# Kernel optimization log

Hardware: AMD Instinct MI355X
Metric: run time of the kernel (lower is better)

## Reference

```python
import jax, jax.numpy as jnp
import numpy as np

# SHOT descriptor hyperparameters (match init_kwargs defaults)
K_LRF = 16        # neighbors_for_lrf
A_BINS = 8        # azimuth bins
E_BINS = 2        # elevation bins
R_BINS = 2        # radial bins
H_BINS = 11       # cosine-histogram bins
EPS = 1e-8


def knn_shot_lrf(vertices, k):
    """vertices: (N,3). Returns lrfs (N,3,3) with column 0 = normal,
    neighborhoods (N,k,3) relative coords, neighbor indices (N,k)."""
    # Pairwise squared distances (N,N) -- dominant memory-bound intermediate.
    d2 = jnp.sum((vertices[:, None, :] - vertices[None, :, :]) ** 2, axis=-1)
    neg_d2, idx = jax.lax.top_k(-d2, k)                 # k nearest (incl. self)
    dists = jnp.sqrt(jnp.maximum(-neg_d2, 0.0))         # (N,k)
    neighborhoods = vertices[idx] - vertices[:, None, :]  # (N,k,3)

    # SHOT local reference frame: distance-weighted covariance + eigh.
    radius = dists[:, -1]                                # (N,) support radius
    w = jnp.maximum(radius[:, None] - dists, 0.0)        # (N,k)
    cov = jnp.einsum('nk,nki,nkj->nij', w, neighborhoods, neighborhoods)
    cov = cov / (jnp.sum(w, axis=-1)[:, None, None] + EPS)
    _, evecs = jnp.linalg.eigh(cov)                      # ascending eigenvalues
    n = evecs[..., 0]                                    # normal: smallest eval
    x = evecs[..., 2]                                    # x-axis: largest eval

    # Sign disambiguation: orient each axis with the majority of neighbors.
    proj_n = jnp.einsum('nki,ni->nk', neighborhoods, n)
    n = n * jnp.where(jnp.sum(jnp.sign(proj_n), axis=-1) >= 0, 1.0, -1.0)[:, None]
    proj_x = jnp.einsum('nki,ni->nk', neighborhoods, x)
    x = x * jnp.where(jnp.sum(jnp.sign(proj_x), axis=-1) >= 0, 1.0, -1.0)[:, None]
    y = jnp.cross(n, x)
    lrfs = jnp.stack([n, x, y], axis=-1)                 # lrfs[..., 0] = normal
    return lrfs, neighborhoods, idx


def shot_descr(neighborhoods, normals, neighborhood_indices, radius):
    """Spherical-grid (azimuth x elevation x radial) histograms of normal cosines."""
    N, k, _ = neighborhoods.shape
    nbr_normals = normals[neighborhood_indices]          # (N,k,3) irregular gather
    cos = jnp.clip(jnp.einsum('ni,nki->nk', normals, nbr_normals), -1.0, 1.0)

    r = jnp.linalg.norm(neighborhoods, axis=-1)          # (N,k)
    xg, yg, zg = neighborhoods[..., 0], neighborhoods[..., 1], neighborhoods[..., 2]

    az = jnp.arctan2(yg, xg)                                             # [-pi, pi]
    az_bin = jnp.clip(((az + jnp.pi) / (2.0 * jnp.pi) * A_BINS).astype(jnp.int32), 0, A_BINS - 1)
    el = (zg / (r + EPS) + 1.0) * 0.5                                    # [0, 1]
    el_bin = jnp.clip((el * E_BINS).astype(jnp.int32), 0, E_BINS - 1)
    rad_bin = jnp.clip((r / (radius + EPS) * R_BINS).astype(jnp.int32), 0, R_BINS - 1)
    h_bin = jnp.clip(((cos + 1.0) * 0.5 * H_BINS).astype(jnp.int32), 0, H_BINS - 1)

    flat = ((az_bin * E_BINS + el_bin) * R_BINS + rad_bin) * H_BINS + h_bin  # (N,k)
    mask = (r <= radius).astype(neighborhoods.dtype)

    total = A_BINS * E_BINS * R_BINS * H_BINS
    descr = jnp.zeros((N, total), neighborhoods.dtype)
    descr = descr.at[jnp.arange(N)[:, None], flat].add(mask)             # scatter-add
    return descr / (jnp.linalg.norm(descr, axis=-1, keepdims=True) + EPS)


def _one_cloud(vertices):
    lrfs, nbh, idx = knn_shot_lrf(vertices, K_LRF)
    # sphere_radius == 0.0 branch: global max neighborhood extent
    radius = jnp.max(jnp.linalg.norm(nbh, axis=-1))
    return shot_descr(nbh, lrfs[..., 0], idx, radius)


def setup_inputs() -> dict:
    key = jax.random.key(0)
    vertices = jax.random.normal(key, (8, 4096, 3), dtype=jnp.float32)
    return {"vertices": vertices}


def reference(vertices):
    # (B, N, 3) -> (B, N, 352)
    return jax.vmap(_one_cloud)(vertices)
```

## Files before the change

### kernel.cpp

```cpp
#include <hip/hip_runtime.h>
#include <math.h>

#define NPTS 4096
#define KNN 16
#define TBINS 352
#define PPB 16
#define CITER (NPTS / 16)
#define CAP 96
#define BINOFF 210
#define HROW 68

__device__ __forceinline__ void ins16(unsigned long long* K, unsigned long long key) {
  if (key < K[15]) {
#pragma unroll
    for (int q = 15; q >= 1; --q) {
      bool ltm = key < K[q - 1];
      bool ltk = key < K[q];
      K[q] = ltm ? K[q - 1] : (ltk ? key : K[q]);
    }
    if (key < K[0]) K[0] = key;
  }
}

#define JROT(App, Aqq, Apq, Arp, Arq, V0p, V0q, V1p, V1q, V2p, V2q)            \
  do {                                                                         \
    double apq_ = Apq;                                                         \
    if (fabs(apq_) > 1e-300) {                                                 \
      double tau_ = (Aqq - App) / (2.0 * apq_);                                \
      double t_ = (tau_ >= 0.0) ? 1.0 / (tau_ + sqrt(1.0 + tau_ * tau_))       \
                                : 1.0 / (tau_ - sqrt(1.0 + tau_ * tau_));      \
      double c_ = 1.0 / sqrt(1.0 + t_ * t_);                                   \
      double s_ = t_ * c_;                                                     \
      App = App - t_ * apq_;                                                   \
      Aqq = Aqq + t_ * apq_;                                                   \
      Apq = 0.0;                                                               \
      double u_, w_;                                                           \
      u_ = Arp; w_ = Arq; Arp = c_ * u_ - s_ * w_; Arq = s_ * u_ + c_ * w_;    \
      u_ = V0p; w_ = V0q; V0p = c_ * u_ - s_ * w_; V0q = s_ * u_ + c_ * w_;    \
      u_ = V1p; w_ = V1q; V1p = c_ * u_ - s_ * w_; V1q = s_ * u_ + c_ * w_;    \
      u_ = V2p; w_ = V2q; V2p = c_ * u_ - s_ * w_; V2q = s_ * u_ + c_ * w_;    \
    }                                                                          \
  } while (0)

__global__ __launch_bounds__(256, 2) void knn_select_kernel(
    const float* __restrict__ verts,
    int* __restrict__ nbr_idx,
    unsigned int* __restrict__ rad2_bits)
{
  __shared__ unsigned char hist[256 * HROW];
  __shared__ unsigned short ptot[PPB][64];
  __shared__ unsigned long long surv[PPB][CAP];
  __shared__ unsigned int scnt[PPB];
  __shared__ unsigned int tbl[PPB];
  __shared__ unsigned int radsh[PPB];

  const int blk = blockIdx.x;
  const int cloud = blk >> 8;
  const int pbase = (blk & 255) * PPB;
  const float* __restrict__ vb = verts + (size_t)cloud * NPTS * 3;
  const int tid = (int)threadIdx.x;

  {
    unsigned int* h32 = (unsigned int*)hist;
#pragma unroll
    for (int k = 0; k < 17; ++k) h32[tid * 17 + k] = 0u;
  }
  if (tid < PPB) scnt[tid] = 0u;
  __syncthreads();

  const int p = tid >> 4;
  const int c = tid & 15;
  const int i = pbase + p;
  const float xi = vb[3 * i + 0], yi = vb[3 * i + 1], zi = vb[3 * i + 2];

#pragma unroll 4
  for (int s = 0; s < CITER; ++s) {
    const int j = (s << 4) | c;
    const float* vp = vb + 3 * j;
    float dx = __fsub_rn(vp[0], xi);
    float dy = __fsub_rn(vp[1], yi);
    float dz = __fsub_rn(vp[2], zi);
    float d2 = __fadd_rn(__fadd_rn(__fmul_rn(dx, dx), __fmul_rn(dy, dy)),
                         __fmul_rn(dz, dz));
    int b = (int)(__float_as_uint(d2) >> 22) - BINOFF;
    b = min(max(b, 0), 63);
    hist[tid * HROW + b] += (unsigned char)1;
  }
  __syncthreads();

#pragma unroll
  for (int bq = 0; bq < 4; ++bq) {
    int b = 4 * c + bq;
    unsigned int tot = 0;
    for (int r = 0; r < 16; ++r) tot += hist[(p * 16 + r) * HROW + b];
    ptot[p][b] = (unsigned short)tot;
  }
  __syncthreads();

  if (c == 0) {
    unsigned int cum = 0; int B = 63;
    for (int b = 0; b < 64; ++b) {
      cum += ptot[p][b];
      if (cum >= KNN) { B = b; break; }
    }
    tbl[p] = (B >= 63) ? 0xFFFFFFFFu : ((unsigned int)(B + 1 + BINOFF) << 22);
  }
  __syncthreads();

  {
    const unsigned int T = tbl[p];
#pragma unroll 4
    for (int s = 0; s < CITER; ++s) {
      const int j = (s << 4) | c;
      const float* vp = vb + 3 * j;
      float dx = __fsub_rn(vp[0], xi);
      float dy = __fsub_rn(vp[1], yi);
      float dz = __fsub_rn(vp[2], zi);
      float d2 = __fadd_rn(__fadd_rn(__fmul_rn(dx, dx), __fmul_rn(dy, dy)),
                           __fmul_rn(dz, dz));
      unsigned int bits = __float_as_uint(d2);
      if (bits < T) {
        unsigned int pos = atomicAdd(&scnt[p], 1u);
        if (pos < CAP) surv[p][pos] = ((unsigned long long)bits << 32) | (unsigned int)j;
      }
    }
  }
  __syncthreads();

  if (c == 0) {
    unsigned long long K[KNN];
#pragma unroll
    for (int k = 0; k < KNN; ++k) K[k] = 0xFFFFFFFFFFFFFFFFull;
    const int n = (int)scnt[p];
    if (n <= CAP) {
      for (int t = 0; t < n; ++t) ins16(K, surv[p][t]);
    } else {
      for (int j = 0; j < NPTS; ++j) {
        const float* vp = vb + 3 * j;
        float dx = __fsub_rn(vp[0], xi);
        float dy = __fsub_rn(vp[1], yi);
        float dz = __fsub_rn(vp[2], zi);
        float d2 = __fadd_rn(__fadd_rn(__fmul_rn(dx, dx), __fmul_rn(dy, dy)),
                             __fmul_rn(dz, dz));
        ins16(K, ((unsigned long long)__float_as_uint(d2) << 32) | (unsigned int)j);
      }
    }
    const int gp = cloud * NPTS + i;
#pragma unroll
    for (int k = 0; k < KNN; ++k) nbr_idx[gp * KNN + k] = (int)(K[k] & 0xFFFFFFFFull);
    radsh[p] = (unsigned int)(K[KNN - 1] >> 32);
  }
  __syncthreads();

  if (tid == 0) {
    unsigned int m = radsh[0];
#pragma unroll
    for (int q = 1; q < PPB; ++q) m = max(m, radsh[q]);
    atomicMax(&rad2_bits[cloud], m);
  }
}

__global__ __launch_bounds__(256, 1) void normal_kernel(
    const float* __restrict__ verts,
    const int* __restrict__ nbr_idx,
    float* __restrict__ normals)
{
  const int t = blockIdx.x * 256 + (int)threadIdx.x;
  const int gp = t >> 4;
  const int c = t & 15;
  const int cloud = gp >> 12;
  const int i = gp & (NPTS - 1);
  const float* __restrict__ vb = verts + (size_t)cloud * NPTS * 3;
  const float xi = vb[3 * i + 0], yi = vb[3 * i + 1], zi = vb[3 * i + 2];

  const int id = nbr_idx[gp * KNN + c];
  const float* vp = vb + 3 * id;
  const float dx = __fsub_rn(vp[0], xi);
  const float dy = __fsub_rn(vp[1], yi);
  const float dz = __fsub_rn(vp[2], zi);
  const float d2 = __fadd_rn(__fadd_rn(__fmul_rn(dx, dx), __fmul_rn(dy, dy)),
                             __fmul_rn(dz, dz));
  const double dist = sqrt((double)d2);
  const double radius_i = __shfl(dist, 15, 16);

  double w = radius_i - dist;
  if (w < 0.0) w = 0.0;
  const double dxd = (double)dx, dyd = (double)dy, dzd = (double)dz;
  const double wx = w * dxd, wy = w * dyd;
  double c00 = wx * dxd, c01 = wx * dyd, c02 = wx * dzd;
  double c11 = wy * dyd, c12 = wy * dzd, c22 = (w * dzd) * dzd;
  double sw = w;

#pragma unroll
  for (int m = 8; m >= 1; m >>= 1) {
    c00 += __shfl_xor(c00, m);
    c01 += __shfl_xor(c01, m);
    c02 += __shfl_xor(c02, m);
    c11 += __shfl_xor(c11, m);
    c12 += __shfl_xor(c12, m);
    c22 += __shfl_xor(c22, m);
    sw  += __shfl_xor(sw,  m);
  }

  const double inv = 1.0 / (sw + 1e-8);
  c00 *= inv; c01 *= inv; c02 *= inv; c11 *= inv; c12 *= inv; c22 *= inv;

  double A00 = c00, A01 = c01, A02 = c02, A11 = c11, A12 = c12, A22 = c22;
  double v00 = 1, v01 = 0, v02 = 0,
         v10 = 0, v11 = 1, v12 = 0,
         v20 = 0, v21 = 0, v22 = 1;
  for (int sweep = 0; sweep < 8; ++sweep) {
    JROT(A00, A11, A01, A02, A12, v00, v01, v10, v11, v20, v21);
    JROT(A00, A22, A02, A01, A12, v00, v02, v10, v12, v20, v22);
    JROT(A11, A22, A12, A01, A02, v01, v02, v11, v12, v21, v22);
  }

  double nx, ny, nz;
  if (A00 <= A11 && A00 <= A22)      { nx = v00; ny = v10; nz = v20; }
  else if (A11 <= A22)               { nx = v01; ny = v11; nz = v21; }
  else                               { nx = v02; ny = v12; nz = v22; }
  const double rn = 1.0 / sqrt(nx * nx + ny * ny + nz * nz);
  nx *= rn; ny *= rn; nz *= rn;

  const double pr = dxd * nx + dyd * ny + dzd * nz;
  int sv = (pr > 0.0) - (pr < 0.0);
#pragma unroll
  for (int m = 8; m >= 1; m >>= 1) sv += __shfl_xor(sv, m);
  if (sv < 0) { nx = -nx; ny = -ny; nz = -nz; }

  if (c == 0) {
    normals[3 * gp + 0] = (float)nx;
    normals[3 * gp + 1] = (float)ny;
    normals[3 * gp + 2] = (float)nz;
  }
}

__global__ __launch_bounds__(256) void bins_kernel(
    const float* __restrict__ verts,
    const float* __restrict__ normals,
    const int* __restrict__ nbr_idx,
    const unsigned int* __restrict__ rad2_bits,
    unsigned short* __restrict__ bins,
    float* __restrict__ denoms)
{
  const int gp = blockIdx.x * 256 + threadIdx.x;
  const int cloud = gp >> 12;
  const int i = gp & (NPTS - 1);
  const float* __restrict__ vb = verts + (size_t)cloud * NPTS * 3;
  const float xi = vb[3 * i + 0], yi = vb[3 * i + 1], zi = vb[3 * i + 2];
  const float nxi = normals[3 * gp + 0];
  const float nyi = normals[3 * gp + 1];
  const float nzi = normals[3 * gp + 2];
  const float radius = (float)sqrt((double)__uint_as_float(rad2_bits[cloud]));
  const float rpe = __fadd_rn(radius, 1e-8f);
  const float PI_F = 3.14159274101257324f;
  const float TWOPI_F = 6.28318548202514648f;

  int bl[KNN];
#pragma unroll
  for (int k = 0; k < KNN; ++k) {
    int j = nbr_idx[gp * KNN + k];
    float dx = __fsub_rn(vb[3 * j + 0], xi);
    float dy = __fsub_rn(vb[3 * j + 1], yi);
    float dz = __fsub_rn(vb[3 * j + 2], zi);
    float d2f = __fadd_rn(__fadd_rn(__fmul_rn(dx, dx), __fmul_rn(dy, dy)),
                          __fmul_rn(dz, dz));
    float r = (float)sqrt((double)d2f);

    float az = (float)atan2((double)dy, (double)dx);
    int azb = (int)__fmul_rn(__fdiv_rn(__fadd_rn(az, PI_F), TWOPI_F), 8.0f);
    azb = min(max(azb, 0), 7);

    float el = __fmul_rn(__fadd_rn(__fdiv_rn(dz, __fadd_rn(r, 1e-8f)), 1.0f), 0.5f);
    int elb = (int)__fmul_rn(el, 2.0f);
    elb = min(max(elb, 0), 1);

    int rb = (int)__fmul_rn(__fdiv_rn(r, rpe), 2.0f);
    rb = min(max(rb, 0), 1);

    int gj = cloud * NPTS + j;
    double cd = (double)nxi * (double)normals[3 * gj + 0] +
                (double)nyi * (double)normals[3 * gj + 1] +
                (double)nzi * (double)normals[3 * gj + 2];
    cd = fmin(fmax(cd, -1.0), 1.0);
    float cf = (float)cd;
    int hb = (int)__fmul_rn(__fmul_rn(__fadd_rn(cf, 1.0f), 0.5f), 11.0f);
    hb = min(max(hb, 0), 10);

    bl[k] = ((azb * 2 + elb) * 2 + rb) * 11 + hb;
  }

  int pairs = 0;
#pragma unroll
  for (int a = 0; a < KNN; ++a)
#pragma unroll
    for (int b = 0; b < KNN; ++b) pairs += (bl[a] == bl[b]) ? 1 : 0;

  denoms[gp] = __fadd_rn(sqrtf((float)pairs), 1e-8f);
  unsigned short* bp = bins + (size_t)gp * KNN;
#pragma unroll
  for (int k = 0; k < KNN; ++k) bp[k] = (unsigned short)bl[k];
}

__global__ __launch_bounds__(256) void out_kernel(
    const unsigned short* __restrict__ bins,
    const float* __restrict__ denoms,
    float* __restrict__ out)
{
  const int gid = blockIdx.x * 256 + threadIdx.x;
  const int p = gid / TBINS;
  const int b = gid - p * TBINS;
  const unsigned short* __restrict__ bp = bins + (size_t)p * KNN;
  int c = 0;
#pragma unroll
  for (int k = 0; k < KNN; ++k) c += (bp[k] == (unsigned short)b) ? 1 : 0;
  out[gid] = __fdiv_rn((float)c, denoms[p]);
}

extern "C" void kernel_launch(void* const* d_in, const int* in_sizes, int n_in,
                              void* d_out, int out_size, void* d_ws, size_t ws_size,
                              hipStream_t stream) {
  const float* verts = (const float*)d_in[0];
  float* out = (float*)d_out;

  char* ws = (char*)d_ws;
  float* normals = (float*)ws;
  int* nidx = (int*)(ws + 393216);
  unsigned short* bins = (unsigned short*)(ws + 2490368);
  float* denoms = (float*)(ws + 3538944);
  unsigned int* radb = (unsigned int*)(ws + 3670016);

  hipMemsetAsync(radb, 0, 8 * sizeof(unsigned int), stream);

  knn_select_kernel<<<2048, 256, 0, stream>>>(verts, nidx, radb);
  normal_kernel<<<2048, 256, 0, stream>>>(verts, nidx, normals);
  bins_kernel<<<128, 256, 0, stream>>>(verts, normals, nidx, radb, bins, denoms);
  const int total = 8 * NPTS * TBINS;
  out_kernel<<<total / 256, 256, 0, stream>>>(bins, denoms, out);
}
```

Before: 319.5 us.

## Pack vertices to float4 and use register-packed coarse histogram for kNN threshold

Adds a pre-pass that packs vertices into float4 so every kernel fetches a point with a single vector load instead of three scalar loads. In the kNN selection kernel, the 64-bin LDS byte histogram keyed on 22-bit float prefixes is replaced with a 16-bin histogram keyed on the float exponent. Each thread accumulates it in 4-bit nibble counters packed into 64-bit registers and flushes them into two 64-bit accumulators, which removes the LDS read-modify-writes and the histogram zeroing. Coarser bins admit more survivors, so CAP rises to 160 to reduce fallback to the full brute-force scan, at the cost of more insertion-sort work per point and one extra small kernel launch.

```diff
diff --git a/kernel.cpp b/kernel.cpp
--- a/kernel.cpp
+++ b/kernel.cpp
@@ -6,9 +6,9 @@
 #define TBINS 352
 #define PPB 16
 #define CITER (NPTS / 16)
-#define CAP 96
-#define BINOFF 210
-#define HROW 68
+#define CAP 160
+#define NBIN 16
+#define OFF23 117
 
 __device__ __forceinline__ void ins16(unsigned long long* K, unsigned long long key) {
   if (key < K[15]) {
@@ -42,13 +42,20 @@
     }                                                                          \
   } while (0)
 
+__global__ __launch_bounds__(256) void pack4_kernel(
+    const float* __restrict__ verts, float4* __restrict__ v4)
+{
+  const int g = blockIdx.x * 256 + (int)threadIdx.x;
+  v4[g] = make_float4(verts[3 * g + 0], verts[3 * g + 1], verts[3 * g + 2], 0.0f);
+}
+
 __global__ __launch_bounds__(256, 2) void knn_select_kernel(
-    const float* __restrict__ verts,
+    const float4* __restrict__ v4,
     int* __restrict__ nbr_idx,
     unsigned int* __restrict__ rad2_bits)
 {
-  __shared__ unsigned char hist[256 * HROW];
-  __shared__ unsigned short ptot[PPB][64];
+  __shared__ unsigned long long hdump[256][2];
+  __shared__ unsigned short ptot[PPB][NBIN];
   __shared__ unsigned long long surv[PPB][CAP];
   __shared__ unsigned int scnt[PPB];
   __shared__ unsigned int tbl[PPB];
@@ -57,53 +64,58 @@
   const int blk = blockIdx.x;
   const int cloud = blk >> 8;
   const int pbase = (blk & 255) * PPB;
-  const float* __restrict__ vb = verts + (size_t)cloud * NPTS * 3;
+  const float4* __restrict__ vb = v4 + ((size_t)cloud << 12);
   const int tid = (int)threadIdx.x;
 
-  {
-    unsigned int* h32 = (unsigned int*)hist;
-#pragma unroll
-    for (int k = 0; k < 17; ++k) h32[tid * 17 + k] = 0u;
-  }
   if (tid < PPB) scnt[tid] = 0u;
-  __syncthreads();
 
   const int p = tid >> 4;
   const int c = tid & 15;
   const int i = pbase + p;
-  const float xi = vb[3 * i + 0], yi = vb[3 * i + 1], zi = vb[3 * i + 2];
-
-#pragma unroll 4
-  for (int s = 0; s < CITER; ++s) {
-    const int j = (s << 4) | c;
-    const float* vp = vb + 3 * j;
-    float dx = __fsub_rn(vp[0], xi);
-    float dy = __fsub_rn(vp[1], yi);
-    float dz = __fsub_rn(vp[2], zi);
-    float d2 = __fadd_rn(__fadd_rn(__fmul_rn(dx, dx), __fmul_rn(dy, dy)),
-                         __fmul_rn(dz, dz));
-    int b = (int)(__float_as_uint(d2) >> 22) - BINOFF;
-    b = min(max(b, 0), 63);
-    hist[tid * HROW + b] += (unsigned char)1;
-  }
-  __syncthreads();
-
-#pragma unroll
-  for (int bq = 0; bq < 4; ++bq) {
-    int b = 4 * c + bq;
+  const float4 me = vb[i];
+  const float xi = me.x, yi = me.y, zi = me.z;
+
+  unsigned long long accA = 0ull, accB = 0ull;
+  for (int s0 = 0; s0 < CITER; s0 += 8) {
+    unsigned long long h4 = 0ull;
+#pragma unroll
+    for (int q = 0; q < 8; ++q) {
+      const int j = ((s0 + q) << 4) | c;
+      const float4 vj = vb[j];
+      float dx = __fsub_rn(vj.x, xi);
+      float dy = __fsub_rn(vj.y, yi);
+      float dz = __fsub_rn(vj.z, zi);
+      float d2 = __fadd_rn(__fadd_rn(__fmul_rn(dx, dx), __fmul_rn(dy, dy)),
+                           __fmul_rn(dz, dz));
+      int b = (int)(__float_as_uint(d2) >> 23) - OFF23;
+      b = min(max(b, 0), NBIN - 1);
+      h4 += 1ull << (b << 2);
+    }
+    accA += h4 & 0x0F0F0F0F0F0F0F0Full;
+    accB += (h4 >> 4) & 0x0F0F0F0F0F0F0F0Full;
+  }
+  hdump[tid][0] = accA;
+  hdump[tid][1] = accB;
+  __syncthreads();
+
+  {
+    const int half = c & 1;
+    const int sh = (c >> 1) << 3;
     unsigned int tot = 0;
-    for (int r = 0; r < 16; ++r) tot += hist[(p * 16 + r) * HROW + b];
-    ptot[p][b] = (unsigned short)tot;
+    for (int r = 0; r < 16; ++r)
+      tot += (unsigned int)((hdump[p * 16 + r][half] >> sh) & 0xFFull);
+    ptot[p][c] = (unsigned short)tot;
   }
   __syncthreads();
 
   if (c == 0) {
-    unsigned int cum = 0; int B = 63;
-    for (int b = 0; b < 64; ++b) {
+    unsigned int cum = 0; int B = NBIN - 1;
+    for (int b = 0; b < NBIN; ++b) {
       cum += ptot[p][b];
       if (cum >= KNN) { B = b; break; }
     }
-    tbl[p] = (B >= 63) ? 0xFFFFFFFFu : ((unsigned int)(B + 1 + BINOFF) << 22);
+    tbl[p] = (B >= NBIN - 1) ? 0xFFFFFFFFu
+                             : ((unsigned int)(B + 1 + OFF23) << 23);
   }
   __syncthreads();
 
@@ -112,10 +124,10 @@
 #pragma unroll 4
     for (int s = 0; s < CITER; ++s) {
       const int j = (s << 4) | c;
-      const float* vp = vb + 3 * j;
-      float dx = __fsub_rn(vp[0], xi);
-      float dy = __fsub_rn(vp[1], yi);
-      float dz = __fsub_rn(vp[2], zi);
+      const float4 vj = vb[j];
+      float dx = __fsub_rn(vj.x, xi);
+      float dy = __fsub_rn(vj.y, yi);
+      float dz = __fsub_rn(vj.z, zi);
       float d2 = __fadd_rn(__fadd_rn(__fmul_rn(dx, dx), __fmul_rn(dy, dy)),
                            __fmul_rn(dz, dz));
       unsigned int bits = __float_as_uint(d2);
@@ -136,10 +148,10 @@
       for (int t = 0; t < n; ++t) ins16(K, surv[p][t]);
     } else {
       for (int j = 0; j < NPTS; ++j) {
-        const float* vp = vb + 3 * j;
-        float dx = __fsub_rn(vp[0], xi);
-        float dy = __fsub_rn(vp[1], yi);
-        float dz = __fsub_rn(vp[2], zi);
+        const float4 vj = vb[j];
+        float dx = __fsub_rn(vj.x, xi);
+        float dy = __fsub_rn(vj.y, yi);
+        float dz = __fsub_rn(vj.z, zi);
         float d2 = __fadd_rn(__fadd_rn(__fmul_rn(dx, dx), __fmul_rn(dy, dy)),
                              __fmul_rn(dz, dz));
         ins16(K, ((unsigned long long)__float_as_uint(d2) << 32) | (unsigned int)j);
@@ -161,7 +173,7 @@
 }
 
 __global__ __launch_bounds__(256, 1) void normal_kernel(
-    const float* __restrict__ verts,
+    const float4* __restrict__ v4,
     const int* __restrict__ nbr_idx,
     float* __restrict__ normals)
 {
@@ -170,14 +182,15 @@
   const int c = t & 15;
   const int cloud = gp >> 12;
   const int i = gp & (NPTS - 1);
-  const float* __restrict__ vb = verts + (size_t)cloud * NPTS * 3;
-  const float xi = vb[3 * i + 0], yi = vb[3 * i + 1], zi = vb[3 * i + 2];
+  const float4* __restrict__ vb = v4 + ((size_t)cloud << 12);
+  const float4 me = vb[i];
+  const float xi = me.x, yi = me.y, zi = me.z;
 
   const int id = nbr_idx[gp * KNN + c];
-  const float* vp = vb + 3 * id;
-  const float dx = __fsub_rn(vp[0], xi);
-  const float dy = __fsub_rn(vp[1], yi);
-  const float dz = __fsub_rn(vp[2], zi);
+  const float4 vj = vb[id];
+  const float dx = __fsub_rn(vj.x, xi);
+  const float dy = __fsub_rn(vj.y, yi);
+  const float dz = __fsub_rn(vj.z, zi);
   const float d2 = __fadd_rn(__fadd_rn(__fmul_rn(dx, dx), __fmul_rn(dy, dy)),
                              __fmul_rn(dz, dz));
   const double dist = sqrt((double)d2);
@@ -236,7 +249,7 @@
 }
 
 __global__ __launch_bounds__(256) void bins_kernel(
-    const float* __restrict__ verts,
+    const float4* __restrict__ v4,
     const float* __restrict__ normals,
     const int* __restrict__ nbr_idx,
     const unsigned int* __restrict__ rad2_bits,
@@ -246,8 +259,9 @@
   const int gp = blockIdx.x * 256 + threadIdx.x;
   const int cloud = gp >> 12;
   const int i = gp & (NPTS - 1);
-  const float* __restrict__ vb = verts + (size_t)cloud * NPTS * 3;
-  const float xi = vb[3 * i + 0], yi = vb[3 * i + 1], zi = vb[3 * i + 2];
+  const float4* __restrict__ vb = v4 + ((size_t)cloud << 12);
+  const float4 me = vb[i];
+  const float xi = me.x, yi = me.y, zi = me.z;
   const float nxi = normals[3 * gp + 0];
   const float nyi = normals[3 * gp + 1];
   const float nzi = normals[3 * gp + 2];
@@ -260,9 +274,10 @@
 #pragma unroll
   for (int k = 0; k < KNN; ++k) {
     int j = nbr_idx[gp * KNN + k];
-    float dx = __fsub_rn(vb[3 * j + 0], xi);
-    float dy = __fsub_rn(vb[3 * j + 1], yi);
-    float dz = __fsub_rn(vb[3 * j + 2], zi);
+    const float4 vj = vb[j];
+    float dx = __fsub_rn(vj.x, xi);
+    float dy = __fsub_rn(vj.y, yi);
+    float dz = __fsub_rn(vj.z, zi);
     float d2f = __fadd_rn(__fadd_rn(__fmul_rn(dx, dx), __fmul_rn(dy, dy)),
                           __fmul_rn(dz, dz));
     float r = (float)sqrt((double)d2f);
@@ -329,12 +344,14 @@
   unsigned short* bins = (unsigned short*)(ws + 2490368);
   float* denoms = (float*)(ws + 3538944);
   unsigned int* radb = (unsigned int*)(ws + 3670016);
+  float4* v4 = (float4*)(ws + 3670048);
 
   hipMemsetAsync(radb, 0, 8 * sizeof(unsigned int), stream);
 
-  knn_select_kernel<<<2048, 256, 0, stream>>>(verts, nidx, radb);
-  normal_kernel<<<2048, 256, 0, stream>>>(verts, nidx, normals);
-  bins_kernel<<<128, 256, 0, stream>>>(verts, normals, nidx, radb, bins, denoms);
+  pack4_kernel<<<128, 256, 0, stream>>>(verts, v4);
+  knn_select_kernel<<<2048, 256, 0, stream>>>(v4, nidx, radb);
+  normal_kernel<<<2048, 256, 0, stream>>>(v4, nidx, normals);
+  bins_kernel<<<128, 256, 0, stream>>>(v4, normals, nidx, radb, bins, denoms);
   const int total = 8 * NPTS * TBINS;
   out_kernel<<<total / 256, 256, 0, stream>>>(bins, denoms, out);
 }
```

New measurement: 705.8 us. +120.9%, slower.
